# Kernel optimization log

Measured on AMD Instinct MI355X. Metric: run time of the kernel, lower is better.

## Reference

```python
import jax, jax.numpy as jnp
import numpy as np

MU = 1.0  # opts.loss_type[1]


def setup_inputs() -> dict:
    key = jax.random.key(0)
    k1, k2 = jax.random.split(key)
    B, D, N = 8, 3, 4096
    srcs = jax.random.normal(k1, (B, D, N), dtype=jnp.float32)
    tgts = jax.random.normal(k2, (B, D, N), dtype=jnp.float32)
    return {"srcs": srcs, "tgts": tgts}


def reference(srcs, tgts):
    # [B, D, N] -> [B, N, D]
    s = jnp.transpose(srcs, (0, 2, 1))
    t = jnp.transpose(tgts, (0, 2, 1))
    # squared euclidean pairwise distances: ||s_i - t_j||^2, [B, N, M]
    s_sq = jnp.sum(s * s, axis=-1)          # [B, N]
    t_sq = jnp.sum(t * t, axis=-1)          # [B, M]
    cross = jnp.einsum('bnd,bmd->bnm', s, t)  # [B, N, M]
    P = s_sq[:, :, None] + t_sq[:, None, :] - 2.0 * cross
    # bidirectional chamfer mins
    d_tgt = jnp.min(P, axis=1)  # min over src points, [B, M]
    d_src = jnp.min(P, axis=2)  # min over tgt points, [B, N]
    distances = jnp.stack([d_tgt, d_src], axis=-1)  # [B, N, 2]
    # Geman-McClure robust penalty
    losses = (MU * distances / (distances + MU)).sum(axis=2).mean(axis=1).mean()
    return losses
```

## Files before the change

### kernel.cpp

```cpp
#include <hip/hip_runtime.h>


#define NPTS 4096
#define NB   8

typedef __attribute__((ext_vector_type(8))) short bf16x8;
typedef __attribute__((ext_vector_type(4))) float floatx4;

#define OFF_APACK_S 0u
#define OFF_APACK_T (1u << 20)
#define OFF_BPACK_S (2u << 20)
#define OFF_BPACK_T (3u << 20)
#define OFF_BSUM    (4u << 20)

union V16 { int4 i; bf16x8 h; };

__device__ __forceinline__ unsigned short f2bf(float f) {
    unsigned u = __float_as_uint(f);
    u += 0x7FFFu + ((u >> 16) & 1u);
    return (unsigned short)(u >> 16);
}
__device__ __forceinline__ float bf2f(unsigned short h) {
    return __uint_as_float(((unsigned)h) << 16);
}
__device__ __forceinline__ int pk(unsigned short lo, unsigned short hi) {
    return (int)((unsigned)lo | ((unsigned)hi << 16));
}

__device__ __forceinline__ void pack_point(const float* __restrict__ cloud,
                                           int b, int j, int gid,
                                           char* __restrict__ apack,
                                           char* __restrict__ bpack) {
    const unsigned short ONE = 0x3F80;
    const float* p = cloud + b * 3 * NPTS;
    const float x = p[j], y = p[NPTS + j], z = p[2 * NPTS + j];
    const unsigned short hx = f2bf(x), hy = f2bf(y), hz = f2bf(z);
    const unsigned short lx = f2bf(x - bf2f(hx));
    const unsigned short ly = f2bf(y - bf2f(hy));
    const unsigned short lz = f2bf(z - bf2f(hz));
    const unsigned short a0 = f2bf(-2.0f * bf2f(hx));
    const unsigned short a1 = f2bf(-2.0f * bf2f(hy));
    const unsigned short a2 = f2bf(-2.0f * bf2f(hz));
    const unsigned short m0 = f2bf(-2.0f * (x - bf2f(hx)));
    const unsigned short m1 = f2bf(-2.0f * (y - bf2f(hy)));
    const unsigned short m2 = f2bf(-2.0f * (z - bf2f(hz)));
    const float n2 = fmaf(z, z, fmaf(y, y, x * x));
    const unsigned short n2h = f2bf(n2);
    const unsigned short n2l = f2bf(n2 - bf2f(n2h));

    int4* Ap = (int4*)(apack + (size_t)gid * 32);
    Ap[0] = make_int4(pk(a0, a1), pk(a2, m0), pk(m1, m2), pk(a0, a1));
    Ap[1] = make_int4(pk(a2, n2h), pk(n2l, ONE), pk(ONE, 0), 0);

    int4* Bp = (int4*)(bpack + (size_t)gid * 32);
    Bp[0] = make_int4(pk(hx, hy), pk(hz, hx), pk(hy, hz), pk(lx, ly));
    Bp[1] = make_int4(pk(lz, ONE), pk(ONE, n2h), pk(n2l, 0), 0);
}

__global__ __launch_bounds__(256)
void transform_kernel(const float* __restrict__ srcs,
                      const float* __restrict__ tgts,
                      char* __restrict__ ws) {
    const int gid = blockIdx.x * 256 + threadIdx.x;
    const int b = gid >> 12, j = gid & 4095;
    pack_point(srcs, b, j, gid, ws + OFF_APACK_S, ws + OFF_BPACK_S);
    pack_point(tgts, b, j, gid, ws + OFF_APACK_T, ws + OFF_BPACK_T);
}

__global__ __launch_bounds__(512, 4)
void chamfer_kernel(char* __restrict__ ws) {
    const int blk    = blockIdx.x;
    const int group  = blk & 15;
    const int dir    = group >> 3;
    const int b      = group & 7;
    const int stripe = blk >> 4;
    const int tid    = threadIdx.x;
    const int wave   = tid >> 6;
    const int lane   = tid & 63;
    const int l15    = lane & 15;
    const int quad   = lane >> 4;

    const char* Ap = ws + (dir == 0 ? OFF_APACK_S : OFF_APACK_T);
    const char* Bp = ws + (dir == 0 ? OFF_BPACK_T : OFF_BPACK_S);

    V16 av0, av1;
    av0.i = *(const int4*)(Ap + (size_t)(b * NPTS + stripe * 32 + l15) * 32 + (quad & 1) * 16);
    av1.i = *(const int4*)(Ap + (size_t)(b * NPTS + stripe * 32 + 16 + l15) * 32 + (quad & 1) * 16);

    floatx4 rmin0 = {3.0e38f, 3.0e38f, 3.0e38f, 3.0e38f};
    floatx4 rmin1 = rmin0;
    const floatx4 zero = {0.0f, 0.0f, 0.0f, 0.0f};

    const int ct0 = wave * 32;
    const char* bbase = Bp + (size_t)(b * NPTS + ct0 * 16 + l15) * 32 + (quad & 1) * 16;

    V16 t0, t1, t2, t3;
    t0.i = *(const int4*)(bbase);
    t1.i = *(const int4*)(bbase + 512);
    t2.i = *(const int4*)(bbase + 1024);
    t3.i = *(const int4*)(bbase + 1536);

#pragma unroll
    for (int i = 0; i < 32; i += 4) {
        V16 n0, n1, n2, n3;
        n0.i = *(const int4*)(bbase + (size_t)((i + 4) & 31) * 512);
        n1.i = *(const int4*)(bbase + (size_t)((i + 5) & 31) * 512);
        n2.i = *(const int4*)(bbase + (size_t)((i + 6) & 31) * 512);
        n3.i = *(const int4*)(bbase + (size_t)((i + 7) & 31) * 512);
#pragma unroll
        for (int u = 0; u < 4; u++) {
            const bf16x8 bf = (u == 0 ? t0.h : u == 1 ? t1.h : u == 2 ? t2.h : t3.h);
            const floatx4 d0 =
                __builtin_amdgcn_mfma_f32_16x16x32_bf16(av0.h, bf, zero, 0, 0, 0);
            const floatx4 d1 =
                __builtin_amdgcn_mfma_f32_16x16x32_bf16(av1.h, bf, zero, 0, 0, 0);
#pragma unroll
            for (int r = 0; r < 4; r++) {
                rmin0[r] = fminf(rmin0[r], d0[r]);
                rmin1[r] = fminf(rmin1[r], d1[r]);
            }
        }
        t0 = n0; t1 = n1; t2 = n2; t3 = n3;
    }

#pragma unroll
    for (int off = 1; off < 16; off <<= 1) {
#pragma unroll
        for (int r = 0; r < 4; r++) {
            rmin0[r] = fminf(rmin0[r], __shfl_xor(rmin0[r], off, 64));
            rmin1[r] = fminf(rmin1[r], __shfl_xor(rmin1[r], off, 64));
        }
    }
    __shared__ float sRow[8][32];
    if (l15 == 0) {
#pragma unroll
        for (int r = 0; r < 4; r++) {
            sRow[wave][quad * 4 + r]      = rmin0[r];
            sRow[wave][16 + quad * 4 + r] = rmin1[r];
        }
    }
    __syncthreads();
    if (tid < 32) {
        float m = 3.0e38f;
#pragma unroll
        for (int w = 0; w < 8; w++) m = fminf(m, sRow[w][tid]);
        m = fmaxf(m * 0.5f, 0.0f);
        float g = m / (m + 1.0f);
#pragma unroll
        for (int off = 1; off < 32; off <<= 1)
            g += __shfl_xor(g, off, 64);
        if (tid == 0)
            ((float*)(ws + OFF_BSUM))[blk] = g;
    }
}

__global__ __launch_bounds__(256)
void finish_kernel(const char* __restrict__ ws, float* __restrict__ out) {
    const float* bsum = (const float*)(ws + OFF_BSUM);
    const int tid = threadIdx.x;
    float g = 0.0f;
#pragma unroll
    for (int k = 0; k < 8; k++) g += bsum[tid + k * 256];
#pragma unroll
    for (int off = 1; off < 64; off <<= 1)
        g += __shfl_xor(g, off, 64);
    __shared__ float sp[4];
    if ((tid & 63) == 0) sp[tid >> 6] = g;
    __syncthreads();
    if (tid == 0)
        out[0] = (sp[0] + sp[1] + sp[2] + sp[3]) * (1.0f / (NB * NPTS));
}

extern "C" void kernel_launch(void* const* d_in, const int* in_sizes, int n_in,
                              void* d_out, int out_size, void* d_ws, size_t ws_size,
                              hipStream_t stream) {
    const float* srcs = (const float*)d_in[0];
    const float* tgts = (const float*)d_in[1];
    float* out = (float*)d_out;
    char* ws = (char*)d_ws;

    transform_kernel<<<dim3(128), dim3(256), 0, stream>>>(srcs, tgts, ws);
    chamfer_kernel<<<dim3(2048), dim3(512), 0, stream>>>(ws);
    finish_kernel<<<dim3(1), dim3(256), 0, stream>>>(ws, out);
}
```

Before: 77.25 us.

## Widen chamfer row tile to 128 points per block to reuse B fragments

Each block now handles 128 query rows (8 MFMA row tiles) instead of 32, so every loaded B fragment of 16 target points feeds 8 MFMAs rather than 2. The grid shrinks from 2048 to 512 blocks, and the block-level reduction and finish kernel are adjusted to match. This cuts global/L2 traffic for the B operand and the per-block launch and reduction overhead, in exchange for more VGPRs per thread (8 A fragments and 8 accumulators) and fewer blocks to spread across the CUs.

```diff
diff --git a/kernel.cpp b/kernel.cpp
--- a/kernel.cpp
+++ b/kernel.cpp
@@ -83,12 +83,16 @@
     const char* Ap = ws + (dir == 0 ? OFF_APACK_S : OFF_APACK_T);
     const char* Bp = ws + (dir == 0 ? OFF_BPACK_T : OFF_BPACK_S);
 
-    V16 av0, av1;
-    av0.i = *(const int4*)(Ap + (size_t)(b * NPTS + stripe * 32 + l15) * 32 + (quad & 1) * 16);
-    av1.i = *(const int4*)(Ap + (size_t)(b * NPTS + stripe * 32 + 16 + l15) * 32 + (quad & 1) * 16);
+    V16 av[8];
+#pragma unroll
+    for (int rt = 0; rt < 8; rt++)
+        av[rt].i = *(const int4*)(Ap +
+            (size_t)(b * NPTS + stripe * 128 + rt * 16 + l15) * 32 + (quad & 1) * 16);
 
-    floatx4 rmin0 = {3.0e38f, 3.0e38f, 3.0e38f, 3.0e38f};
-    floatx4 rmin1 = rmin0;
+    floatx4 rmin[8];
+#pragma unroll
+    for (int rt = 0; rt < 8; rt++)
+        rmin[rt] = (floatx4){3.0e38f, 3.0e38f, 3.0e38f, 3.0e38f};
     const floatx4 zero = {0.0f, 0.0f, 0.0f, 0.0f};
 
     const int ct0 = wave * 32;
@@ -110,14 +114,13 @@
 #pragma unroll
         for (int u = 0; u < 4; u++) {
             const bf16x8 bf = (u == 0 ? t0.h : u == 1 ? t1.h : u == 2 ? t2.h : t3.h);
-            const floatx4 d0 =
-                __builtin_amdgcn_mfma_f32_16x16x32_bf16(av0.h, bf, zero, 0, 0, 0);
-            const floatx4 d1 =
-                __builtin_amdgcn_mfma_f32_16x16x32_bf16(av1.h, bf, zero, 0, 0, 0);
 #pragma unroll
-            for (int r = 0; r < 4; r++) {
-                rmin0[r] = fminf(rmin0[r], d0[r]);
-                rmin1[r] = fminf(rmin1[r], d1[r]);
+            for (int rt = 0; rt < 8; rt++) {
+                const floatx4 d =
+                    __builtin_amdgcn_mfma_f32_16x16x32_bf16(av[rt].h, bf, zero, 0, 0, 0);
+#pragma unroll
+                for (int r = 0; r < 4; r++)
+                    rmin[rt][r] = fminf(rmin[rt][r], d[r]);
             }
         }
         t0 = n0; t1 = n1; t2 = n2; t3 = n3;
@@ -126,41 +129,42 @@
 #pragma unroll
     for (int off = 1; off < 16; off <<= 1) {
 #pragma unroll
-        for (int r = 0; r < 4; r++) {
-            rmin0[r] = fminf(rmin0[r], __shfl_xor(rmin0[r], off, 64));
-            rmin1[r] = fminf(rmin1[r], __shfl_xor(rmin1[r], off, 64));
-        }
+        for (int rt = 0; rt < 8; rt++)
+#pragma unroll
+            for (int r = 0; r < 4; r++)
+                rmin[rt][r] = fminf(rmin[rt][r], __shfl_xor(rmin[rt][r], off, 64));
     }
-    __shared__ float sRow[8][32];
+    __shared__ float sRow[8][128];
+    __shared__ float sRed[2];
     if (l15 == 0) {
 #pragma unroll
-        for (int r = 0; r < 4; r++) {
-            sRow[wave][quad * 4 + r]      = rmin0[r];
-            sRow[wave][16 + quad * 4 + r] = rmin1[r];
-        }
+        for (int rt = 0; rt < 8; rt++)
+#pragma unroll
+            for (int r = 0; r < 4; r++)
+                sRow[wave][rt * 16 + quad * 4 + r] = rmin[rt][r];
     }
     __syncthreads();
-    if (tid < 32) {
+    if (tid < 128) {
         float m = 3.0e38f;
 #pragma unroll
         for (int w = 0; w < 8; w++) m = fminf(m, sRow[w][tid]);
         m = fmaxf(m * 0.5f, 0.0f);
         float g = m / (m + 1.0f);
 #pragma unroll
-        for (int off = 1; off < 32; off <<= 1)
+        for (int off = 1; off < 64; off <<= 1)
             g += __shfl_xor(g, off, 64);
-        if (tid == 0)
-            ((float*)(ws + OFF_BSUM))[blk] = g;
+        if ((tid & 63) == 0) sRed[tid >> 6] = g;
     }
+    __syncthreads();
+    if (tid == 0)
+        ((float*)(ws + OFF_BSUM))[blk] = sRed[0] + sRed[1];
 }
 
 __global__ __launch_bounds__(256)
 void finish_kernel(const char* __restrict__ ws, float* __restrict__ out) {
     const float* bsum = (const float*)(ws + OFF_BSUM);
     const int tid = threadIdx.x;
-    float g = 0.0f;
-#pragma unroll
-    for (int k = 0; k < 8; k++) g += bsum[tid + k * 256];
+    float g = bsum[tid] + bsum[tid + 256];
 #pragma unroll
     for (int off = 1; off < 64; off <<= 1)
         g += __shfl_xor(g, off, 64);
@@ -180,6 +184,6 @@
     char* ws = (char*)d_ws;
 
     transform_kernel<<<dim3(128), dim3(256), 0, stream>>>(srcs, tgts, ws);
-    chamfer_kernel<<<dim3(2048), dim3(512), 0, stream>>>(ws);
+    chamfer_kernel<<<dim3(512), dim3(512), 0, stream>>>(ws);
     finish_kernel<<<dim3(1), dim3(256), 0, stream>>>(ws, out);
 }
```

Result: slower. 159.1 us (+106.0%).
